# Optimization experiments

Measured on AMD Instinct MI355X. Metric: run time of the kernel, lower is better.

The kernel has to match this reference:

```python
import jax, jax.numpy as jnp
from jax import lax
import numpy as np

SEQ, BATCH, IN_SIZE = 512, 256, 58
HIDDEN = 256
N_LAYERS = 2
N_CAT = 18


def setup_inputs() -> dict:
    key = jax.random.key(0)
    ks = jax.random.split(key, 12)
    s = 1.0 / np.sqrt(HIDDEN)
    u = lambda k, shape: jax.random.uniform(k, shape, jnp.float32, -s, s)
    return {
        "x": jax.random.normal(ks[0], (SEQ, BATCH, IN_SIZE), jnp.float32),
        "W_ih0": u(ks[1], (3 * HIDDEN, IN_SIZE)),
        "W_hh0": u(ks[2], (3 * HIDDEN, HIDDEN)),
        "b_ih0": u(ks[3], (3 * HIDDEN,)),
        "b_hh0": u(ks[4], (3 * HIDDEN,)),
        "W_ih1": u(ks[5], (3 * HIDDEN, HIDDEN)),
        "W_hh1": u(ks[6], (3 * HIDDEN, HIDDEN)),
        "b_ih1": u(ks[7], (3 * HIDDEN,)),
        "b_hh1": u(ks[8], (3 * HIDDEN,)),
        "fc_w": u(ks[9], (N_CAT, HIDDEN)),
        "fc_b": u(ks[10], (N_CAT,)),
    }


def gru_layer(x, W_ih, W_hh, b_ih, b_hh):
    # x: (T, B, I). PyTorch GRU gate order: r, z, n.
    H = W_hh.shape[1]
    gx = jnp.einsum('tbi,gi->tbg', x, W_ih) + b_ih  # precompute input gates (T,B,3H)

    def step(h, gx_t):
        gh = h @ W_hh.T + b_hh                      # (B, 3H)
        r = jax.nn.sigmoid(gx_t[:, :H] + gh[:, :H])
        z = jax.nn.sigmoid(gx_t[:, H:2 * H] + gh[:, H:2 * H])
        n = jnp.tanh(gx_t[:, 2 * H:] + r * gh[:, 2 * H:])
        h_new = (1.0 - z) * n + z * h
        return h_new, h_new

    h0 = jnp.zeros((x.shape[1], H), x.dtype)
    _, out = lax.scan(step, h0, gx)                 # out: (T, B, H)
    return out


def reference(x, W_ih0, W_hh0, b_ih0, b_hh0, W_ih1, W_hh1, b_ih1, b_hh1, fc_w, fc_b):
    h = gru_layer(x, W_ih0, W_hh0, b_ih0, b_hh0)
    h = gru_layer(h, W_ih1, W_hh1, b_ih1, b_hh1)
    # final linear on last timestep only: (B, H) @ (H, C) + (C,)
    return h[-1] @ fc_w.T + fc_b
```

## Files before the change

### kernel.cpp

```cpp
#include <hip/hip_runtime.h>

typedef _Float16 f16;
typedef _Float16 f16x2 __attribute__((ext_vector_type(2)));
typedef _Float16 f16x8 __attribute__((ext_vector_type(8)));
typedef float f32x4 __attribute__((ext_vector_type(4)));
typedef unsigned int u32;

#define SEQ   512
#define BATCH 256
#define INS   58
#define INP   64
#define HID   256
#define NCAT  18
#define G3    (3*HID)
#define TC    128
#define NCHUNK (SEQ/TC)
#define MC    (TC*BATCH)

__device__ __forceinline__ float fdot2f(u32 a, u32 b, float c) {
#if __has_builtin(__builtin_amdgcn_fdot2)
  return __builtin_amdgcn_fdot2(__builtin_bit_cast(f16x2, a),
                                __builtin_bit_cast(f16x2, b), c, false);
#else
  f16x2 av = __builtin_bit_cast(f16x2, a);
  f16x2 bv = __builtin_bit_cast(f16x2, b);
  return c + (float)av[0] * (float)bv[0] + (float)av[1] * (float)bv[1];
#endif
}

__global__ void k_convert_pad(const float* __restrict__ src, f16* __restrict__ dst,
                              int rows, int scols, int dcols) {
  int i = blockIdx.x * blockDim.x + threadIdx.x;
  int total = rows * dcols;
  if (i >= total) return;
  int r = i / dcols, c = i - r * dcols;
  float v = (c < scols) ? src[(size_t)r * scols + c] : 0.f;
  dst[i] = (f16)v;
}

#define BM 128
#define BN 128
#define BK 32
#define LDP 40

__global__ __launch_bounds__(256, 2)
void k_gemm_f16(const f16* __restrict__ A, const f16* __restrict__ W,
                const float* __restrict__ bias, f16* __restrict__ out,
                int K) {
  __shared__ __align__(16) f16 As[BM][LDP];
  __shared__ __align__(16) f16 Ws[BN][LDP];
  const int tid  = threadIdx.x;
  const int lane = tid & 63;
  const int wave = tid >> 6;
  const int wm = wave >> 1, wn = wave & 1;
  const int n0 = blockIdx.x * BN;
  const int m0 = blockIdx.y * BM;

  f32x4 acc[4][4] = {};

  for (int k0 = 0; k0 < K; k0 += BK) {
    __syncthreads();
#pragma unroll
    for (int c = 0; c < 2; ++c) {
      int j   = c * 256 + tid;
      int row = j >> 2;
      int kc  = j & 3;
      uint4 va = *(const uint4*)(A + (size_t)(m0 + row) * K + k0 + kc * 8);
      *(uint4*)(&As[row][kc * 8]) = va;
      uint4 vw = *(const uint4*)(W + (size_t)(n0 + row) * K + k0 + kc * 8);
      *(uint4*)(&Ws[row][kc * 8]) = vw;
    }
    __syncthreads();
    const int rsel = lane & 15;
    const int ks   = (lane >> 4) * 8;
    f16x8 af[4], bf[4];
#pragma unroll
    for (int i = 0; i < 4; ++i)
      af[i] = *(const f16x8*)(&As[wm * 64 + i * 16 + rsel][ks]);
#pragma unroll
    for (int j = 0; j < 4; ++j)
      bf[j] = *(const f16x8*)(&Ws[wn * 64 + j * 16 + rsel][ks]);
#pragma unroll
    for (int i = 0; i < 4; ++i)
#pragma unroll
      for (int j = 0; j < 4; ++j)
        acc[i][j] = __builtin_amdgcn_mfma_f32_16x16x32_f16(af[i], bf[j], acc[i][j], 0, 0, 0);
  }

#pragma unroll
  for (int j = 0; j < 4; ++j) {
    int col = n0 + wn * 64 + j * 16 + (lane & 15);
    float bv = bias[col];
#pragma unroll
    for (int i = 0; i < 4; ++i) {
      int rbase = m0 + wm * 64 + i * 16 + ((lane >> 4) << 2);
#pragma unroll
      for (int rr = 0; rr < 4; ++rr)
        out[(size_t)(rbase + rr) * G3 + col] = (f16)(acc[i][j][rr] + bv);
    }
  }
}

template <int FINAL>
__global__ __launch_bounds__(512, 2)
void k_gru(const f16* __restrict__ gx,
           const f16* __restrict__ Whh,
           const float* __restrict__ bhh,
           f16* __restrict__ hout,
           float* __restrict__ hstate,
           int first, int last,
           const float* __restrict__ fcw,
           const float* __restrict__ fcb,
           float* __restrict__ out) {
  const int b   = blockIdx.x;
  const int tid = threadIdx.x;
  const int r   = tid >> 1;
  const int kh  = tid & 1;

  __shared__ __align__(16) f16 hsh[2][HID];
  __shared__ float red[HID];
  __shared__ float red2[NCAT * 16];

  u32 w0[64], w1[64], w2[64];
  {
    const f16* base = Whh + (size_t)kh * 128;
#pragma unroll
    for (int c = 0; c < 16; ++c) {
      uint4 v0 = *(const uint4*)(base + (size_t)(0 * HID + r) * HID + c * 8);
      w0[c * 4 + 0] = v0.x; w0[c * 4 + 1] = v0.y; w0[c * 4 + 2] = v0.z; w0[c * 4 + 3] = v0.w;
      uint4 v1 = *(const uint4*)(base + (size_t)(1 * HID + r) * HID + c * 8);
      w1[c * 4 + 0] = v1.x; w1[c * 4 + 1] = v1.y; w1[c * 4 + 2] = v1.z; w1[c * 4 + 3] = v1.w;
      uint4 v2 = *(const uint4*)(base + (size_t)(2 * HID + r) * HID + c * 8);
      w2[c * 4 + 0] = v2.x; w2[c * 4 + 1] = v2.y; w2[c * 4 + 2] = v2.z; w2[c * 4 + 3] = v2.w;
    }
  }
#pragma unroll
  for (int i = 0; i < 64; ++i)
    asm volatile("" : "+v"(w0[i]), "+v"(w1[i]), "+v"(w2[i]));

  float bhr = 0.f, bhz = 0.f, bhn = 0.f;
  float hprev = 0.f;
  if (kh == 0) {
    bhr = bhh[r]; bhz = bhh[HID + r]; bhn = bhh[2 * HID + r];
    hprev = first ? 0.f : hstate[(size_t)b * HID + r];
    hsh[0][r] = (f16)hprev;
  }

  float gxr = 0.f, gxz = 0.f, gxn = 0.f;
  if (kh == 0) {
    const f16* g0 = gx + ((size_t)0 * BATCH + b) * G3;
    gxr = (float)g0[r]; gxz = (float)g0[HID + r]; gxn = (float)g0[2 * HID + r];
  }
  __syncthreads();

  int cur = 0;
  for (int t = 0; t < TC; ++t) {
    float nxr = 0.f, nxz = 0.f, nxn = 0.f;
    if (kh == 0 && t + 1 < TC) {
      const f16* gn = gx + ((size_t)(t + 1) * BATCH + b) * G3;
      nxr = (float)gn[r]; nxz = (float)gn[HID + r]; nxn = (float)gn[2 * HID + r];
    }

    float ar = 0.f, az = 0.f, an = 0.f;
    const uint4* hp = (const uint4*)(&hsh[cur][kh * 128]);
#pragma unroll
    for (int c = 0; c < 16; ++c) {
      uint4 v = hp[c];
      ar = fdot2f(w0[c * 4 + 0], v.x, ar);
      az = fdot2f(w1[c * 4 + 0], v.x, az);
      an = fdot2f(w2[c * 4 + 0], v.x, an);
      ar = fdot2f(w0[c * 4 + 1], v.y, ar);
      az = fdot2f(w1[c * 4 + 1], v.y, az);
      an = fdot2f(w2[c * 4 + 1], v.y, an);
      ar = fdot2f(w0[c * 4 + 2], v.z, ar);
      az = fdot2f(w1[c * 4 + 2], v.z, az);
      an = fdot2f(w2[c * 4 + 2], v.z, an);
      ar = fdot2f(w0[c * 4 + 3], v.w, ar);
      az = fdot2f(w1[c * 4 + 3], v.w, az);
      an = fdot2f(w2[c * 4 + 3], v.w, an);
    }
    ar += __shfl_xor(ar, 1);
    az += __shfl_xor(az, 1);
    an += __shfl_xor(an, 1);

    if (kh == 0) {
      float ghr = ar + bhr;
      float ghz = az + bhz;
      float ghn = an + bhn;
      float rg = 1.f / (1.f + __expf(-(gxr + ghr)));
      float zg = 1.f / (1.f + __expf(-(gxz + ghz)));
      float nt = gxn + rg * ghn;
      float e2 = __expf(-2.f * fabsf(nt));
      float th = (1.f - e2) / (1.f + e2);
      float ng = (nt >= 0.f) ? th : -th;
      float hn = (1.f - zg) * ng + zg * hprev;
      hprev = hn;
      hsh[cur ^ 1][r] = (f16)hn;
      if (!FINAL) hout[((size_t)t * BATCH + b) * HID + r] = (f16)hn;
      gxr = nxr; gxz = nxz; gxn = nxn;
    }
    __syncthreads();
    cur ^= 1;
  }

  if (kh == 0) hstate[(size_t)b * HID + r] = hprev;

  if (FINAL) {
    if (last) {
      if (kh == 0) red[r] = hprev;
      __syncthreads();
      int c = tid >> 4, seg = tid & 15;
      if (c < NCAT) {
        const float* wrow = fcw + (size_t)c * HID + seg * 16;
        const float* hseg = red + seg * 16;
        float s = 0.f;
#pragma unroll
        for (int q = 0; q < 16; ++q) s += wrow[q] * hseg[q];
        red2[c * 16 + seg] = s;
      }
      __syncthreads();
      if (tid < NCAT) {
        float s = fcb[tid];
#pragma unroll
        for (int k = 0; k < 16; ++k) s += red2[tid * 16 + k];
        out[(size_t)b * NCAT + tid] = s;
      }
    }
  }
}

extern "C" void kernel_launch(void* const* d_in, const int* in_sizes, int n_in,
                              void* d_out, int out_size, void* d_ws, size_t ws_size,
                              hipStream_t stream) {
  const float* x    = (const float*)d_in[0];
  const float* Wih0 = (const float*)d_in[1];
  const float* Whh0 = (const float*)d_in[2];
  const float* bih0 = (const float*)d_in[3];
  const float* bhh0 = (const float*)d_in[4];
  const float* Wih1 = (const float*)d_in[5];
  const float* Whh1 = (const float*)d_in[6];
  const float* bih1 = (const float*)d_in[7];
  const float* bhh1 = (const float*)d_in[8];
  const float* fcw  = (const float*)d_in[9];
  const float* fcb  = (const float*)d_in[10];
  float* out = (float*)d_out;

  char* ws = (char*)d_ws;
  size_t off = 0;
  f16*   whh0h = (f16*)(ws + off); off += (size_t)G3 * HID * 2;
  f16*   whh1h = (f16*)(ws + off); off += (size_t)G3 * HID * 2;
  f16*   wih0h = (f16*)(ws + off); off += (size_t)G3 * INP * 2;
  f16*   wih1h = (f16*)(ws + off); off += (size_t)G3 * HID * 2;
  float* h0st  = (float*)(ws + off); off += (size_t)BATCH * HID * 4;
  float* h1st  = (float*)(ws + off); off += (size_t)BATCH * HID * 4;
  f16*   xhc   = (f16*)(ws + off); off += (size_t)MC * INP * 2;
  f16*   h0c   = (f16*)(ws + off); off += (size_t)MC * HID * 2;
  f16*   gxc   = (f16*)(ws + off); off += (size_t)MC * G3 * 2;

  k_convert_pad<<<(G3 * INP + 255) / 256, 256, 0, stream>>>(Wih0, wih0h, G3, INS, INP);
  k_convert_pad<<<(G3 * HID + 255) / 256, 256, 0, stream>>>(Whh0, whh0h, G3, HID, HID);
  k_convert_pad<<<(G3 * HID + 255) / 256, 256, 0, stream>>>(Wih1, wih1h, G3, HID, HID);
  k_convert_pad<<<(G3 * HID + 255) / 256, 256, 0, stream>>>(Whh1, whh1h, G3, HID, HID);

  for (int c = 0; c < NCHUNK; ++c) {
    int first = (c == 0), last = (c == NCHUNK - 1);
    const float* xc = x + (size_t)c * MC * INS;

    k_convert_pad<<<(MC * INP + 255) / 256, 256, 0, stream>>>(xc, xhc, MC, INS, INP);
    k_gemm_f16<<<dim3(G3 / BN, MC / BM), 256, 0, stream>>>(xhc, wih0h, bih0, gxc, INP);
    k_gru<0><<<BATCH, 512, 0, stream>>>(gxc, whh0h, bhh0, h0c, h0st, first, last,
                                        nullptr, nullptr, nullptr);
    k_gemm_f16<<<dim3(G3 / BN, MC / BM), 256, 0, stream>>>(h0c, wih1h, bih1, gxc, HID);
    k_gru<1><<<BATCH, 512, 0, stream>>>(gxc, whh1h, bhh1, nullptr, h1st, first, last,
                                        fcw, fcb, out);
  }
}
```

Before: 1.790 ms.

## Use one thread per hidden unit in GRU recurrence, dropping split-K shuffle

```diff
diff --git a/kernel.cpp b/kernel.cpp
--- a/kernel.cpp
+++ b/kernel.cpp
@@ -102,7 +102,7 @@
 }
 
 template <int FINAL>
-__global__ __launch_bounds__(512, 2)
+__global__ __launch_bounds__(256, 1)
 void k_gru(const f16* __restrict__ gx,
            const f16* __restrict__ Whh,
            const float* __restrict__ bhh,
@@ -114,57 +114,51 @@
            float* __restrict__ out) {
   const int b   = blockIdx.x;
   const int tid = threadIdx.x;
-  const int r   = tid >> 1;
-  const int kh  = tid & 1;
 
   __shared__ __align__(16) f16 hsh[2][HID];
   __shared__ float red[HID];
-  __shared__ float red2[NCAT * 16];
-
-  u32 w0[64], w1[64], w2[64];
+  __shared__ float red2[NCAT * 8];
+
+  u32 w0[128], w1[128], w2[128];
   {
-    const f16* base = Whh + (size_t)kh * 128;
-#pragma unroll
-    for (int c = 0; c < 16; ++c) {
-      uint4 v0 = *(const uint4*)(base + (size_t)(0 * HID + r) * HID + c * 8);
+    const uint4* p0 = (const uint4*)(Whh + (size_t)(0 * HID + tid) * HID);
+    const uint4* p1 = (const uint4*)(Whh + (size_t)(1 * HID + tid) * HID);
+    const uint4* p2 = (const uint4*)(Whh + (size_t)(2 * HID + tid) * HID);
+#pragma unroll
+    for (int c = 0; c < 32; ++c) {
+      uint4 v0 = p0[c];
       w0[c * 4 + 0] = v0.x; w0[c * 4 + 1] = v0.y; w0[c * 4 + 2] = v0.z; w0[c * 4 + 3] = v0.w;
-      uint4 v1 = *(const uint4*)(base + (size_t)(1 * HID + r) * HID + c * 8);
+      uint4 v1 = p1[c];
       w1[c * 4 + 0] = v1.x; w1[c * 4 + 1] = v1.y; w1[c * 4 + 2] = v1.z; w1[c * 4 + 3] = v1.w;
-      uint4 v2 = *(const uint4*)(base + (size_t)(2 * HID + r) * HID + c * 8);
+      uint4 v2 = p2[c];
       w2[c * 4 + 0] = v2.x; w2[c * 4 + 1] = v2.y; w2[c * 4 + 2] = v2.z; w2[c * 4 + 3] = v2.w;
     }
   }
-#pragma unroll
-  for (int i = 0; i < 64; ++i)
-    asm volatile("" : "+v"(w0[i]), "+v"(w1[i]), "+v"(w2[i]));
-
-  float bhr = 0.f, bhz = 0.f, bhn = 0.f;
-  float hprev = 0.f;
-  if (kh == 0) {
-    bhr = bhh[r]; bhz = bhh[HID + r]; bhn = bhh[2 * HID + r];
-    hprev = first ? 0.f : hstate[(size_t)b * HID + r];
-    hsh[0][r] = (f16)hprev;
-  }
-
-  float gxr = 0.f, gxz = 0.f, gxn = 0.f;
-  if (kh == 0) {
-    const f16* g0 = gx + ((size_t)0 * BATCH + b) * G3;
-    gxr = (float)g0[r]; gxz = (float)g0[HID + r]; gxn = (float)g0[2 * HID + r];
-  }
+
+  const float bhr = bhh[tid];
+  const float bhz = bhh[HID + tid];
+  const float bhn = bhh[2 * HID + tid];
+  float hprev = first ? 0.f : hstate[(size_t)b * HID + tid];
+  hsh[0][tid] = (f16)hprev;
+
+  const f16* g0 = gx + ((size_t)0 * BATCH + b) * G3;
+  float gxr = (float)g0[tid];
+  float gxz = (float)g0[HID + tid];
+  float gxn = (float)g0[2 * HID + tid];
   __syncthreads();
 
   int cur = 0;
   for (int t = 0; t < TC; ++t) {
     float nxr = 0.f, nxz = 0.f, nxn = 0.f;
-    if (kh == 0 && t + 1 < TC) {
+    if (t + 1 < TC) {
       const f16* gn = gx + ((size_t)(t + 1) * BATCH + b) * G3;
-      nxr = (float)gn[r]; nxz = (float)gn[HID + r]; nxn = (float)gn[2 * HID + r];
+      nxr = (float)gn[tid]; nxz = (float)gn[HID + tid]; nxn = (float)gn[2 * HID + tid];
     }
 
     float ar = 0.f, az = 0.f, an = 0.f;
-    const uint4* hp = (const uint4*)(&hsh[cur][kh * 128]);
-#pragma unroll
-    for (int c = 0; c < 16; ++c) {
+    const uint4* hp = (const uint4*)(&hsh[cur][0]);
+#pragma unroll
+    for (int c = 0; c < 32; ++c) {
       uint4 v = hp[c];
       ar = fdot2f(w0[c * 4 + 0], v.x, ar);
       az = fdot2f(w1[c * 4 + 0], v.x, az);
@@ -179,50 +173,46 @@
       az = fdot2f(w1[c * 4 + 3], v.w, az);
       an = fdot2f(w2[c * 4 + 3], v.w, an);
     }
-    ar += __shfl_xor(ar, 1);
-    az += __shfl_xor(az, 1);
-    an += __shfl_xor(an, 1);
-
-    if (kh == 0) {
-      float ghr = ar + bhr;
-      float ghz = az + bhz;
-      float ghn = an + bhn;
-      float rg = 1.f / (1.f + __expf(-(gxr + ghr)));
-      float zg = 1.f / (1.f + __expf(-(gxz + ghz)));
-      float nt = gxn + rg * ghn;
-      float e2 = __expf(-2.f * fabsf(nt));
-      float th = (1.f - e2) / (1.f + e2);
-      float ng = (nt >= 0.f) ? th : -th;
-      float hn = (1.f - zg) * ng + zg * hprev;
-      hprev = hn;
-      hsh[cur ^ 1][r] = (f16)hn;
-      if (!FINAL) hout[((size_t)t * BATCH + b) * HID + r] = (f16)hn;
-      gxr = nxr; gxz = nxz; gxn = nxn;
-    }
+
+    float ghr = ar + bhr;
+    float ghz = az + bhz;
+    float ghn = an + bhn;
+    float rg = 1.f / (1.f + __expf(-(gxr + ghr)));
+    float zg = 1.f / (1.f + __expf(-(gxz + ghz)));
+    float nt = gxn + rg * ghn;
+    float e2 = __expf(-2.f * fabsf(nt));
+    float th = (1.f - e2) / (1.f + e2);
+    float ng = (nt >= 0.f) ? th : -th;
+    float hn = (1.f - zg) * ng + zg * hprev;
+    hprev = hn;
+    hsh[cur ^ 1][tid] = (f16)hn;
+    if (!FINAL) hout[((size_t)t * BATCH + b) * HID + tid] = (f16)hn;
+    gxr = nxr; gxz = nxz; gxn = nxn;
+
     __syncthreads();
     cur ^= 1;
   }
 
-  if (kh == 0) hstate[(size_t)b * HID + r] = hprev;
+  hstate[(size_t)b * HID + tid] = hprev;
 
   if (FINAL) {
     if (last) {
-      if (kh == 0) red[r] = hprev;
+      red[tid] = hprev;
       __syncthreads();
-      int c = tid >> 4, seg = tid & 15;
+      int c = tid >> 3, seg = tid & 7;
       if (c < NCAT) {
-        const float* wrow = fcw + (size_t)c * HID + seg * 16;
-        const float* hseg = red + seg * 16;
+        const float* wrow = fcw + (size_t)c * HID + seg * 32;
+        const float* hseg = red + seg * 32;
         float s = 0.f;
 #pragma unroll
-        for (int q = 0; q < 16; ++q) s += wrow[q] * hseg[q];
-        red2[c * 16 + seg] = s;
+        for (int q = 0; q < 32; ++q) s += wrow[q] * hseg[q];
+        red2[c * 8 + seg] = s;
       }
       __syncthreads();
       if (tid < NCAT) {
         float s = fcb[tid];
 #pragma unroll
-        for (int k = 0; k < 16; ++k) s += red2[tid * 16 + k];
+        for (int k = 0; k < 8; ++k) s += red2[tid * 8 + k];
         out[(size_t)b * NCAT + tid] = s;
       }
     }
@@ -259,8 +249,8 @@
 
   k_convert_pad<<<(G3 * INP + 255) / 256, 256, 0, stream>>>(Wih0, wih0h, G3, INS, INP);
   k_convert_pad<<<(G3 * HID + 255) / 256, 256, 0, stream>>>(Whh0, whh0h, G3, HID, HID);
+  k_convert_pad<<<(G3 * HID + 255) / 256, 256, 0, stream>>>(Whh1, whh1h, G3, HID, HID);
   k_convert_pad<<<(G3 * HID + 255) / 256, 256, 0, stream>>>(Wih1, wih1h, G3, HID, HID);
-  k_convert_pad<<<(G3 * HID + 255) / 256, 256, 0, stream>>>(Whh1, whh1h, G3, HID, HID);
 
   for (int c = 0; c < NCHUNK; ++c) {
     int first = (c == 0), last = (c == NCHUNK - 1);
@@ -268,10 +258,10 @@
 
     k_convert_pad<<<(MC * INP + 255) / 256, 256, 0, stream>>>(xc, xhc, MC, INS, INP);
     k_gemm_f16<<<dim3(G3 / BN, MC / BM), 256, 0, stream>>>(xhc, wih0h, bih0, gxc, INP);
-    k_gru<0><<<BATCH, 512, 0, stream>>>(gxc, whh0h, bhh0, h0c, h0st, first, last,
+    k_gru<0><<<BATCH, 256, 0, stream>>>(gxc, whh0h, bhh0, h0c, h0st, first, last,
                                         nullptr, nullptr, nullptr);
     k_gemm_f16<<<dim3(G3 / BN, MC / BM), 256, 0, stream>>>(h0c, wih1h, bih1, gxc, HID);
-    k_gru<1><<<BATCH, 512, 0, stream>>>(gxc, whh1h, bhh1, nullptr, h1st, first, last,
+    k_gru<1><<<BATCH, 256, 0, stream>>>(gxc, whh1h, bhh1, nullptr, h1st, first, last,
                                         fcw, fcb, out);
   }
 }
```

New measurement: 2.854 ms. 1.6x slower.
